# Performance work log

Measured on AMD Instinct MI355X. Metric: run time of the kernel, lower is better.

## Reference

```python
import jax, jax.numpy as jnp
import numpy as np

B, S, T, H, NH, NL = 16, 128, 64, 128, 8, 4
DH = H // NH
FF = 2 * H
SCALE = 1.0 / float(np.sqrt(DH))


def _ln(x, s, b):
    m = x.mean(-1, keepdims=True)
    v = ((x - m) ** 2).mean(-1, keepdims=True)
    return (x - m) * jax.lax.rsqrt(v + 1e-5) * s + b


def _block(x, mask, p):
    Wq, bq, Wk, bk, Wv, bv, Wo, bo, s1, c1, W1, d1, W2, d2, s2, c2 = p
    N, L, _ = x.shape
    q = (x @ Wq + bq).reshape(N, L, NH, DH)
    k = (x @ Wk + bk).reshape(N, L, NH, DH)
    v = (x @ Wv + bv).reshape(N, L, NH, DH)
    scores = jnp.einsum('nqhd,nkhd->nhqk', q, k) * SCALE
    scores = jnp.where(mask[:, None, :, :], scores, -1e9)
    a = jax.nn.softmax(scores, axis=-1)
    o = jnp.einsum('nhqk,nkhd->nqhd', a, v).reshape(N, L, H)
    x = _ln(x + o @ Wo + bo, s1, c1)
    h = jax.nn.relu(x @ W1 + d1)
    return _ln(x + h @ W2 + d2, s2, c2)


def setup_inputs():
    key = jax.random.key(0)
    ks = jax.random.split(key, 16)
    g = lambda k, shape: jax.random.normal(k, shape, jnp.float32) * 0.02
    return {
        'polylines': jax.random.normal(ks[0], (B, S, T, H), jnp.float32),
        'lengths': jax.random.randint(ks[1], (B, S), 0, T + 1),
        'proj_w': g(ks[2], (H, H)), 'proj_b': jnp.zeros((H,), jnp.float32),
        'proj_ln_s': jnp.ones((H,), jnp.float32), 'proj_ln_b': jnp.zeros((H,), jnp.float32),
        'pos_emb': g(ks[3], (1, T, H)),
        'Wq': g(ks[4], (NL, H, H)), 'bq': jnp.zeros((NL, H), jnp.float32),
        'Wk': g(ks[5], (NL, H, H)), 'bk': jnp.zeros((NL, H), jnp.float32),
        'Wv': g(ks[6], (NL, H, H)), 'bv': jnp.zeros((NL, H), jnp.float32),
        'Wo': g(ks[7], (NL, H, H)), 'bo': jnp.zeros((NL, H), jnp.float32),
        'ln1_s': jnp.ones((NL, H), jnp.float32), 'ln1_b': jnp.zeros((NL, H), jnp.float32),
        'W1': g(ks[8], (NL, H, FF)), 'b1': jnp.zeros((NL, FF), jnp.float32),
        'W2': g(ks[9], (NL, FF, H)), 'b2': jnp.zeros((NL, H), jnp.float32),
        'ln2_s': jnp.ones((NL, H), jnp.float32), 'ln2_b': jnp.zeros((NL, H), jnp.float32),
    }


def reference(polylines, lengths, proj_w, proj_b, proj_ln_s, proj_ln_b, pos_emb,
              Wq, bq, Wk, bk, Wv, bv, Wo, bo, ln1_s, ln1_b, W1, b1, W2, b2, ln2_s, ln2_b):
    # valid[b,s,t] = t < lengths[b,s]; lengths==0 -> polyline absent (fully padded)
    valid = jnp.arange(T)[None, None, :] < lengths[:, :, None]  # [B,S,T]
    x = jnp.where(valid[..., None], polylines, -1.0)            # -1 pad as in np.pad(constant_values=-1)
    # mask_temporal[b,s] = outer(valid[b,s], valid[b,s])
    mask_t = (valid[:, :, :, None] & valid[:, :, None, :]).reshape(B * S, T, T)
    # mask_spatial[b,t] = outer(valid[b,:,t], valid[b,:,t])
    vs = jnp.transpose(valid, (0, 2, 1))                        # [B,T,S]
    mask_s = (vs[:, :, :, None] & vs[:, :, None, :]).reshape(B * T, S, S)

    x = x.reshape(B * S, T, H)
    x = jax.nn.relu(_ln(x @ proj_w + proj_b, proj_ln_s, proj_ln_b))  # MLP: Linear->LN->ReLU
    x = x + pos_emb[:, :T, :]

    mask = mask_t
    for i in range(NL):
        if i == NL // 2:
            # switch from temporal to spatial attention: [B*S,T,H] -> [B*T,S,H]
            x = x.reshape(B, S, T, H).transpose(0, 2, 1, 3).reshape(B * T, S, H)
            mask = mask_s
        p = (Wq[i], bq[i], Wk[i], bk[i], Wv[i], bv[i], Wo[i], bo[i],
             ln1_s[i], ln1_b[i], W1[i], b1[i], W2[i], b2[i], ln2_s[i], ln2_b[i])
        x = _block(x, mask, p)
    # faithful to original final reshape (treats [B*T,S,H] buffer as [B,S,T,H])
    return x.reshape(B, S, T, H)[:, 0, :]
```

## Files before the change

### kernel.cpp

```cpp
#include <hip/hip_runtime.h>
#include <hip/hip_cooperative_groups.h>

namespace cg = cooperative_groups;

typedef short short8 __attribute__((ext_vector_type(8)));
typedef short short4_t __attribute__((ext_vector_type(4)));
typedef float floatx4 __attribute__((ext_vector_type(4)));
typedef unsigned short ushort_t;

#define B_ 16
#define S_ 128
#define T_ 64
#define H_ 128
#define FF_ 256
#define SCALEQK 0.25f

#define OFFP 0
#define OFFQ(l) (16384 + (l) * 65536)
#define OFFK(l) (OFFQ(l) + 16384)
#define OFFV(l) (OFFQ(l) + 32768)
#define OFFO(l) (OFFQ(l) + 49152)
#define OFFW1(l) (278528 + (l) * 65536)
#define OFFW2(l) (OFFW1(l) + 32768)

__device__ __forceinline__ float b2f(ushort_t u) {
    union { unsigned int i; float f; } x; x.i = ((unsigned int)u) << 16; return x.f;
}
__device__ __forceinline__ ushort_t f2b(float f) {
    union { float f; unsigned int i; } x; x.f = f;
    unsigned int r = x.i + 0x7fffu + ((x.i >> 16) & 1u);
    return (ushort_t)(r >> 16);
}
__device__ __forceinline__ int pack2b(float a, float b) {
    return (int)f2b(a) | ((int)f2b(b) << 16);
}

struct WtEnt { const float* src; int N; int K; int nclog2; int dstoff; };
struct WtArgs { WtEnt e[25]; };

__global__ __launch_bounds__(256) void wt_kernel(WtArgs a, ushort_t* __restrict__ dst) {
    WtEnt ent = a.e[blockIdx.x];
    const int tiles_c = ent.N >> 5;
    const int nt = (ent.K >> 5) * tiles_c;
    const int t = blockIdx.y;
    if (t >= nt) return;
    const int tc = t & (tiles_c - 1);
    const int tr = t >> ent.nclog2;
    __shared__ float ld[32 * 33];
    const int tid = threadIdx.x;
#pragma unroll
    for (int i = 0; i < 4; ++i) {
        int e = tid + i * 256;
        int rr = e >> 5, cc = e & 31;
        ld[rr * 33 + cc] = ent.src[(tr * 32 + rr) * ent.N + tc * 32 + cc];
    }
    __syncthreads();
    ushort_t* d = dst + ent.dstoff;
#pragma unroll
    for (int i = 0; i < 4; ++i) {
        int e = tid + i * 256;
        int rr = e >> 5, cc = e & 31;
        d[(tc * 32 + rr) * ent.K + tr * 32 + cc] = f2b(ld[cc * 33 + rr]);
    }
}

template<int RT, int CT, int KK>
__device__ __forceinline__ void mm_g(const ushort_t* aL, int sa,
                                     const ushort_t* __restrict__ wT,
                                     int colbase, int lane, floatx4 (&acc)[RT][CT]) {
    const int l15 = lane & 15, lq8 = (lane >> 4) * 8;
#pragma unroll
    for (int r = 0; r < RT; ++r)
#pragma unroll
        for (int c = 0; c < CT; ++c) acc[r][c] = (floatx4){0.f, 0.f, 0.f, 0.f};
#pragma unroll
    for (int k0 = 0; k0 < KK; k0 += 32) {
        short8 b[CT];
#pragma unroll
        for (int c = 0; c < CT; ++c)
            b[c] = *(const short8*)&wT[(colbase + c * 16 + l15) * KK + k0 + lq8];
#pragma unroll
        for (int r = 0; r < RT; ++r) {
            short8 a = *(const short8*)&aL[(r * 16 + l15) * sa + k0 + lq8];
#pragma unroll
            for (int c = 0; c < CT; ++c)
                acc[r][c] = __builtin_amdgcn_mfma_f32_16x16x32_bf16(a, b[c], acc[r][c], 0, 0, 0);
        }
    }
}

template<int RT, int CT>
__device__ __forceinline__ void add_bias(floatx4 (&acc)[RT][CT], const float* b,
                                         int colbase, int l15) {
#pragma unroll
    for (int c = 0; c < CT; ++c) {
        float bc = b[colbase + c * 16 + l15];
#pragma unroll
        for (int r = 0; r < RT; ++r)
#pragma unroll
            for (int g = 0; g < 4; ++g) acc[r][c][g] += bc;
    }
}

template<int RT, int CT>
__device__ __forceinline__ void add_resid_reg(floatx4 (&acc)[RT][CT],
                                              const float (&res)[RT][CT][4]) {
#pragma unroll
    for (int r = 0; r < RT; ++r)
#pragma unroll
        for (int c = 0; c < CT; ++c)
#pragma unroll
            for (int g = 0; g < 4; ++g) acc[r][c][g] += res[r][c][g];
}
template<int RT, int CT>
__device__ __forceinline__ void save_resid(float (&res)[RT][CT][4],
                                           const floatx4 (&acc)[RT][CT]) {
#pragma unroll
    for (int r = 0; r < RT; ++r)
#pragma unroll
        for (int c = 0; c < CT; ++c)
#pragma unroll
            for (int g = 0; g < 4; ++g) res[r][c][g] = acc[r][c][g];
}

template<int RT, int CT>
__device__ __forceinline__ void st_n(const floatx4 (&acc)[RT][CT], ushort_t* dst, int stride,
                                     int colbase, int l15, int lq) {
#pragma unroll
    for (int r = 0; r < RT; ++r)
#pragma unroll
        for (int g = 0; g < 4; ++g) {
            int row = r * 16 + lq * 4 + g;
#pragma unroll
            for (int c = 0; c < CT; ++c)
                dst[row * stride + colbase + c * 16 + l15] = f2b(acc[r][c][g]);
        }
}

template<int RT, int CT>
__device__ __forceinline__ void st_t(const floatx4 (&acc)[RT][CT], ushort_t* dst, int stride,
                                     int colbase, int l15, int lq) {
#pragma unroll
    for (int r = 0; r < RT; ++r)
#pragma unroll
        for (int c = 0; c < CT; ++c) {
            int d = colbase + c * 16 + l15;
            short4_t p;
#pragma unroll
            for (int g = 0; g < 4; ++g) p[g] = (short)f2b(acc[r][c][g]);
            *(short4_t*)&dst[d * stride + r * 16 + lq * 4] = p;
        }
}

template<int RT, int CT>
__device__ __forceinline__ void ln_norm(floatx4 (&acc)[RT][CT], float* redL,
                                        const float* lns, const float* lnb,
                                        int colbase, int l15, int lq, int wv) {
#pragma unroll
    for (int r = 0; r < RT; ++r)
#pragma unroll
        for (int g = 0; g < 4; ++g) {
            float s = 0.f, q = 0.f;
#pragma unroll
            for (int c = 0; c < CT; ++c) { float v = acc[r][c][g]; s += v; q += v * v; }
            s += __shfl_xor(s, 1); s += __shfl_xor(s, 2); s += __shfl_xor(s, 4); s += __shfl_xor(s, 8);
            q += __shfl_xor(q, 1); q += __shfl_xor(q, 2); q += __shfl_xor(q, 4); q += __shfl_xor(q, 8);
            if (l15 == 0) {
                int row = r * 16 + lq * 4 + g;
                redL[row * 8 + wv] = s;
                redL[row * 8 + 4 + wv] = q;
            }
        }
    __syncthreads();
#pragma unroll
    for (int r = 0; r < RT; ++r)
#pragma unroll
        for (int g = 0; g < 4; ++g) {
            int row = r * 16 + lq * 4 + g;
            float4 S = *(float4*)&redL[row * 8];
            float4 Q = *(float4*)&redL[row * 8 + 4];
            float mean = (S.x + S.y + S.z + S.w) * (1.f / 128.f);
            float var = (Q.x + Q.y + Q.z + Q.w) * (1.f / 128.f) - mean * mean;
            float rstd = rsqrtf(var + 1e-5f);
#pragma unroll
            for (int c = 0; c < CT; ++c) {
                int col = colbase + c * 16 + l15;
                acc[r][c][g] = (acc[r][c][g] - mean) * rstd * lns[col] + lnb[col];
            }
        }
}

template<int JT>
__device__ __forceinline__ void softmax_pack(floatx4 (&st)[JT], bool iv, unsigned jm,
                                             int (&px)[JT][2]) {
    float ev[JT][4];
    float mx = -3.0e38f;
#pragma unroll
    for (int jt = 0; jt < JT; ++jt)
#pragma unroll
        for (int g = 0; g < 4; ++g) {
            bool ok = iv && ((jm >> (jt * 4 + g)) & 1u);
            float s = ok ? st[jt][g] * SCALEQK : -1e9f;
            ev[jt][g] = s; mx = fmaxf(mx, s);
        }
    mx = fmaxf(mx, __shfl_xor(mx, 16)); mx = fmaxf(mx, __shfl_xor(mx, 32));
    float sum = 0.f;
#pragma unroll
    for (int jt = 0; jt < JT; ++jt)
#pragma unroll
        for (int g = 0; g < 4; ++g) { float e = __expf(ev[jt][g] - mx); ev[jt][g] = e; sum += e; }
    sum += __shfl_xor(sum, 16); sum += __shfl_xor(sum, 32);
    float inv = 1.f / sum;
#pragma unroll
    for (int jt = 0; jt < JT; ++jt) {
        px[jt][0] = pack2b(ev[jt][0] * inv, ev[jt][1] * inv);
        px[jt][1] = pack2b(ev[jt][2] * inv, ev[jt][3] * inv);
    }
}

__device__ __forceinline__ short8 pfrag(const int (*px)[2], int jc, int lq, int l15) {
    const int jA = (lq & 1) * 32 + l15;
    int a0 = __shfl(px[jc * 2][0], jA);
    int a1 = __shfl(px[jc * 2][1], jA);
    int a2 = __shfl(px[jc * 2][0], jA + 16);
    int a3 = __shfl(px[jc * 2][1], jA + 16);
    int b0 = __shfl(px[jc * 2 + 1][0], jA);
    int b1 = __shfl(px[jc * 2 + 1][1], jA);
    int b2 = __shfl(px[jc * 2 + 1][0], jA + 16);
    int b3 = __shfl(px[jc * 2 + 1][1], jA + 16);
    const bool t = (lq >> 1) != 0;
    union { int4 i; short8 s; } u;
    u.i = make_int4(t ? b0 : a0, t ? b1 : a1, t ? b2 : a2, t ? b3 : a3);
    return u.s;
}
__device__ __forceinline__ short8 vfrag(const ushort_t* vT, int stride, int row, int off) {
    int2 a = *(const int2*)&vT[row * stride + off];
    int2 b = *(const int2*)&vT[row * stride + off + 4];
    union { int4 i; short8 s; } u;
    u.i = make_int4(a.x, a.y, b.x, b.y);
    return u.s;
}

__global__ __launch_bounds__(256, 2) void k1_mega(
    const float* __restrict__ poly, const int* __restrict__ lens,
    const ushort_t* __restrict__ wt,
    const float* __restrict__ projb, const float* __restrict__ pls,
    const float* __restrict__ plb, const float* __restrict__ pos,
    const float* __restrict__ bq0, const float* __restrict__ bk0,
    const float* __restrict__ bv0, const float* __restrict__ bo0,
    const float* __restrict__ l1s0, const float* __restrict__ l1b0,
    const float* __restrict__ b10, const float* __restrict__ b20,
    const float* __restrict__ l2s0, const float* __restrict__ l2b0,
    const float* __restrict__ bq1, const float* __restrict__ bk1,
    const float* __restrict__ bv1,
    ushort_t* __restrict__ o1, float* __restrict__ xr0f)
{
    __shared__ ushort_t pool[34816];
    __shared__ float redL[512];
    __shared__ float psL[8 * 68];
    __shared__ float q1L[128];
    ushort_t* xL = pool;
    ushort_t* qL = pool + 8704;
    ushort_t* kL = pool + 17408;
    ushort_t* vT = pool + 26112;
    ushort_t* hL = pool + 17408;

    const int tid = threadIdx.x, lane = tid & 63, wv = tid >> 6;
    const int l15 = lane & 15, lq = lane >> 4;
    const int gid = blockIdx.x;
    const int len = lens[gid];

    {
        const float* pg = poly + (size_t)gid * 8192;
#pragma unroll
        for (int it = 0; it < 8; ++it) {
            int e4 = (tid + it * 256) * 4;
            int row = e4 >> 7, col = e4 & 127;
            float4 f = *(const float4*)(pg + e4);
            if (row >= len) { f.x = -1.f; f.y = -1.f; f.z = -1.f; f.w = -1.f; }
            short4_t u;
            u[0] = (short)f2b(f.x); u[1] = (short)f2b(f.y);
            u[2] = (short)f2b(f.z); u[3] = (short)f2b(f.w);
            *(short4_t*)&xL[row * 136 + col] = u;
        }
    }
    __syncthreads();

    floatx4 a2[4][2];
    float xre[4][2][4];

    mm_g<4, 2, 128>(xL, 136, wt + OFFP, wv * 32, lane, a2);
    add_bias<4, 2>(a2, projb, wv * 32, l15);
    ln_norm<4, 2>(a2, redL, pls, plb, wv * 32, l15, lq, wv);
    __syncthreads();
#pragma unroll
    for (int r = 0; r < 4; ++r)
#pragma unroll
        for (int gg = 0; gg < 4; ++gg) {
            int row = r * 16 + lq * 4 + gg;
#pragma unroll
            for (int c = 0; c < 2; ++c) {
                int col = wv * 32 + c * 16 + l15;
                float v = fmaxf(a2[r][c][gg], 0.f) + pos[row * 128 + col];
                xre[r][c][gg] = v;
                xL[row * 136 + col] = f2b(v);
            }
        }
    __syncthreads();

    mm_g<4, 2, 128>(xL, 136, wt + OFFQ(0), wv * 32, lane, a2);
    add_bias<4, 2>(a2, bq0, wv * 32, l15);
    st_n<4, 2>(a2, qL, 136, wv * 32, l15, lq);
    mm_g<4, 2, 128>(xL, 136, wt + OFFK(0), wv * 32, lane, a2);
    add_bias<4, 2>(a2, bk0, wv * 32, l15);
    st_n<4, 2>(a2, kL, 136, wv * 32, l15, lq);
    mm_g<4, 2, 128>(xL, 136, wt + OFFV(0), wv * 32, lane, a2);
    add_bias<4, 2>(a2, bv0, wv * 32, l15);
    st_t<4, 2>(a2, vT, 68, wv * 32, l15, lq);
    __syncthreads();

    {
        const int iRow = wv * 16 + l15;
        const bool iv = iRow < len;
        unsigned jm = 0;
#pragma unroll
        for (int jt = 0; jt < 4; ++jt)
#pragma unroll
            for (int gg = 0; gg < 4; ++gg)
                if (jt * 16 + lq * 4 + gg < len) jm |= (1u << (jt * 4 + gg));
        for (int h = 0; h < 8; ++h) {
            const int hc = h * 16;
            short8 z8 = {0, 0, 0, 0, 0, 0, 0, 0};
            short8 bqf = z8;
            if (lq < 2) bqf = *(const short8*)&qL[iRow * 136 + hc + lq * 8];
            floatx4 st[4];
#pragma unroll
            for (int jt = 0; jt < 4; ++jt) {
                short8 ak = z8;
                if (lq < 2) ak = *(const short8*)&kL[(jt * 16 + l15) * 136 + hc + lq * 8];
                floatx4 zz = {0.f, 0.f, 0.f, 0.f};
                st[jt] = __builtin_amdgcn_mfma_f32_16x16x32_bf16(ak, bqf, zz, 0, 0, 0);
            }
            int px[4][2];
            softmax_pack<4>(st, iv, jm, px);
            floatx4 ao = {0.f, 0.f, 0.f, 0.f};
#pragma unroll
            for (int jc = 0; jc < 2; ++jc) {
                short8 av = vfrag(vT, 68, hc + l15, jc * 32 + lq * 8);
                short8 bp = pfrag(px, jc, lq, l15);
                ao = __builtin_amdgcn_mfma_f32_16x16x32_bf16(av, bp, ao, 0, 0, 0);
            }
            short4_t w;
#pragma unroll
            for (int gg = 0; gg < 4; ++gg) w[gg] = (short)f2b(ao[gg]);
            *(short4_t*)&qL[iRow * 136 + hc + lq * 4] = w;
        }
    }
    __syncthreads();

    mm_g<4, 2, 128>(qL, 136, wt + OFFO(0), wv * 32, lane, a2);
    add_bias<4, 2>(a2, bo0, wv * 32, l15);
    add_resid_reg<4, 2>(a2, xre);
    ln_norm<4, 2>(a2, redL, l1s0, l1b0, wv * 32, l15, lq, wv);
    save_resid<4, 2>(xre, a2);
    st_n<4, 2>(a2, xL, 136, wv * 32, l15, lq);
    __syncthreads();

    {
        floatx4 a4[4][4];
        mm_g<4, 4, 128>(xL, 136, wt + OFFW1(0), wv * 64, lane, a4);
        add_bias<4, 4>(a4, b10, wv * 64, l15);
#pragma unroll
        for (int r = 0; r < 4; ++r)
#pragma unroll
            for (int c = 0; c < 4; ++c)
#pragma unroll
                for (int gg = 0; gg < 4; ++gg) a4[r][c][gg] = fmaxf(a4[r][c][gg], 0.f);
        st_n<4, 4>(a4, hL, 272, wv * 64, l15, lq);
    }
    __syncthreads();

    mm_g<4, 2, 256>(hL, 272, wt + OFFW2(0), wv * 32, lane, a2);
    add_bias<4, 2>(a2, b20, wv * 32, l15);
    add_resid_reg<4, 2>(a2, xre);
    ln_norm<4, 2>(a2, redL, l2s0, l2b0, wv * 32, l15, lq, wv);
    save_resid<4, 2>(xre, a2);
    st_n<4, 2>(a2, xL, 136, wv * 32, l15, lq);
    if (lq == 0) {
#pragma unroll
        for (int c = 0; c < 2; ++c)
            xr0f[(size_t)gid * 128 + wv * 32 + c * 16 + l15] = a2[0][c][0];
    }
    __syncthreads();

    mm_g<4, 2, 128>(xL, 136, wt + OFFK(1), wv * 32, lane, a2);
    add_bias<4, 2>(a2, bk1, wv * 32, l15);
    st_n<4, 2>(a2, kL, 136, wv * 32, l15, lq);
    mm_g<4, 2, 128>(xL, 136, wt + OFFV(1), wv * 32, lane, a2);
    add_bias<4, 2>(a2, bv1, wv * 32, l15);
    st_t<4, 2>(a2, vT, 68, wv * 32, l15, lq);
    if (tid < 128) {
        int d = tid;
        float a = bq1[d];
        const ushort_t* wq = wt + OFFQ(1) + d * 128;
#pragma unroll 4
        for (int j0 = 0; j0 < 128; j0 += 8) {
            short8 w8 = *(const short8*)&wq[j0];
            short8 x8 = *(const short8*)&xL[j0];
#pragma unroll
            for (int q = 0; q < 8; ++q)
                a = fmaf(b2f((ushort_t)x8[q]), b2f((ushort_t)w8[q]), a);
        }
        q1L[d] = a;
    }
    __syncthreads();

    {
        int h = tid >> 5, jj = tid & 31;
        int hc = h * 16;
        float s[2];
#pragma unroll
        for (int half = 0; half < 2; ++half) {
            int j = jj + half * 32;
            float a = 0.f;
            short8 k0v = *(const short8*)&kL[j * 136 + hc];
            short8 k1v = *(const short8*)&kL[j * 136 + hc + 8];
#pragma unroll
            for (int q = 0; q < 8; ++q) {
                a = fmaf(q1L[hc + q], b2f((ushort_t)k0v[q]), a);
                a = fmaf(q1L[hc + 8 + q], b2f((ushort_t)k1v[q]), a);
            }
            s[half] = (j < len) ? a * SCALEQK : -1e9f;
        }
        float mx = fmaxf(s[0], s[1]);
#pragma unroll
        for (int d = 1; d < 32; d <<= 1) mx = fmaxf(mx, __shfl_xor(mx, d));
        float e0 = __expf(s[0] - mx), e1 = __expf(s[1] - mx);
        float sum = e0 + e1;
#pragma unroll
        for (int d = 1; d < 32; d <<= 1) sum += __shfl_xor(sum, d);
        float inv = 1.f / sum;
        psL[h * 68 + jj] = e0 * inv;
        psL[h * 68 + jj + 32] = e1 * inv;
    }
    __syncthreads();
    if (tid < 128) {
        int h = tid >> 4, d = tid & 15, hc = h * 16;
        float a = 0.f;
#pragma unroll 4
        for (int j0 = 0; j0 < 64; j0 += 4) {
            float4 p4 = *(const float4*)&psL[h * 68 + j0];
            short4_t v4 = *(const short4_t*)&vT[(hc + d) * 68 + j0];
            a += p4.x * b2f((ushort_t)v4[0]) + p4.y * b2f((ushort_t)v4[1])
               + p4.z * b2f((ushort_t)v4[2]) + p4.w * b2f((ushort_t)v4[3]);
        }
        o1[(size_t)gid * 128 + hc + d] = f2b(a);
    }
}

__device__ __forceinline__ void k2a_body(char* smem, int blk,
    const ushort_t* __restrict__ xg, const int* __restrict__ lens,
    const ushort_t* __restrict__ wt, int l,
    const float* __restrict__ bq, const float* __restrict__ bk,
    const float* __restrict__ bv,
    ushort_t* __restrict__ aob)
{
    ushort_t* xL = (ushort_t*)(smem);
    ushort_t* qL = (ushort_t*)(smem + 34816);
    ushort_t* kL = (ushort_t*)(smem + 40960);
    ushort_t* vT = (ushort_t*)(smem + 47104);
    int* vldL = (int*)(smem + 51456);

    const int tid = threadIdx.x, lane = tid & 63, wv = tid >> 6;
    const int l15 = lane & 15, lq = lane >> 4;
    const int g = blk >> 3, h = blk & 7, hc = h * 16;
    const size_t rowg = (size_t)g * 128;

#pragma unroll
    for (int it = 0; it < 8; ++it) {
        int e8 = tid + it * 256;
        int row = e8 >> 4, kg = e8 & 15;
        *(short8*)&xL[row * 136 + kg * 8] = *(const short8*)&xg[(rowg + row) * 128 + kg * 8];
    }
    if (tid < 128) vldL[tid] = (lens[g * 128 + tid] > 0) ? 1 : 0;
    __syncthreads();

    unsigned jm = 0;
#pragma unroll
    for (int jt = 0; jt < 8; ++jt)
#pragma unroll
        for (int gg = 0; gg < 4; ++gg)
            if (vldL[jt * 16 + lq * 4 + gg]) jm |= (1u << (jt * 4 + gg));

    {
        floatx4 a1[2][1];
        mm_g<2, 1, 128>(xL + (wv * 32) * 136, 136, wt + OFFQ(l), hc, lane, a1);
        add_bias<2, 1>(a1, bq, hc, l15);
        st_n<2, 1>(a1, qL + (wv * 32) * 24, 24, 0, l15, lq);
        mm_g<2, 1, 128>(xL + (wv * 32) * 136, 136, wt + OFFK(l), hc, lane, a1);
        add_bias<2, 1>(a1, bk, hc, l15);
        st_n<2, 1>(a1, kL + (wv * 32) * 24, 24, 0, l15, lq);
        mm_g<2, 1, 128>(xL + (wv * 32) * 136, 136, wt + OFFV(l), hc, lane, a1);
        add_bias<2, 1>(a1, bv, hc, l15);
        st_t<2, 1>(a1, vT + wv * 32, 136, 0, l15, lq);
    }
    __syncthreads();

    for (int u = 0; u < 2; ++u) {
        const int iRow = wv * 32 + u * 16 + l15;
        const bool iv = vldL[iRow] != 0;
        short8 z8 = {0, 0, 0, 0, 0, 0, 0, 0};
        short8 bqf = z8;
        if (lq < 2) bqf = *(const short8*)&qL[iRow * 24 + lq * 8];
        floatx4 st[8];
#pragma unroll
        for (int jt = 0; jt < 8; ++jt) {
            short8 ak = z8;
            if (lq < 2) ak = *(const short8*)&kL[(jt * 16 + l15) * 24 + lq * 8];
            floatx4 zz = {0.f, 0.f, 0.f, 0.f};
            st[jt] = __builtin_amdgcn_mfma_f32_16x16x32_bf16(ak, bqf, zz, 0, 0, 0);
        }
        int px[8][2];
        softmax_pack<8>(st, iv, jm, px);
        floatx4 ao = {0.f, 0.f, 0.f, 0.f};
#pragma unroll
        for (int jc = 0; jc < 4; ++jc) {
            short8 av = vfrag(vT, 136, l15, jc * 32 + lq * 8);
            short8 bp = pfrag(px, jc, lq, l15);
            ao = __builtin_amdgcn_mfma_f32_16x16x32_bf16(av, bp, ao, 0, 0, 0);
        }
        short4_t w;
#pragma unroll
        for (int gg = 0; gg < 4; ++gg) w[gg] = (short)f2b(ao[gg]);
        *(short4_t*)&aob[(rowg + iRow) * 128 + hc + lq * 4] = w;
    }
}

template<bool FINAL>
__device__ __forceinline__ void k2b_body(char* smem, int blk,
    const ushort_t* __restrict__ ain, float* __restrict__ xr,
    const ushort_t* __restrict__ wt, int l,
    const float* bo_l, const float* l1s_l, const float* l1b_l,
    const float* b1_l, const float* b2_l, const float* l2s_l, const float* l2b_l,
    ushort_t* __restrict__ xg, float* __restrict__ outp)
{
    ushort_t* aL = (ushort_t*)(smem);
    ushort_t* hL = (ushort_t*)(smem + 4352);
    float* redL = (float*)(smem + 13056);

    const int tid = threadIdx.x, lane = tid & 63, wv = tid >> 6;
    const int l15 = lane & 15, lq = lane >> 4;
    const size_t rowbase = FINAL ? ((size_t)(blk >> 2) * 128 + (blk & 3) * 16)
                                 : ((size_t)blk * 16);

    {
        int row = tid >> 4, kg = tid & 15;
        *(short8*)&aL[row * 136 + kg * 8] = *(const short8*)&ain[(rowbase + row) * 128 + kg * 8];
    }
    __syncthreads();

    floatx4 a2[1][2];
    float xre[1][2][4];

    mm_g<1, 2, 128>(aL, 136, wt + OFFO(l), wv * 32, lane, a2);
    add_bias<1, 2>(a2, bo_l, wv * 32, l15);
#pragma unroll
    for (int c = 0; c < 2; ++c)
#pragma unroll
        for (int gg = 0; gg < 4; ++gg)
            a2[0][c][gg] += xr[(rowbase + lq * 4 + gg) * 128 + wv * 32 + c * 16 + l15];
    ln_norm<1, 2>(a2, redL, l1s_l, l1b_l, wv * 32, l15, lq, wv);
    save_resid<1, 2>(xre, a2);
    st_n<1, 2>(a2, aL, 136, wv * 32, l15, lq);
    __syncthreads();

    {
        floatx4 a4[1][4];
        mm_g<1, 4, 128>(aL, 136, wt + OFFW1(l), wv * 64, lane, a4);
        add_bias<1, 4>(a4, b1_l, wv * 64, l15);
#pragma unroll
        for (int c = 0; c < 4; ++c)
#pragma unroll
            for (int gg = 0; gg < 4; ++gg) a4[0][c][gg] = fmaxf(a4[0][c][gg], 0.f);
        st_n<1, 4>(a4, hL, 272, wv * 64, l15, lq);
    }
    __syncthreads();

    mm_g<1, 2, 256>(hL, 272, wt + OFFW2(l), wv * 32, lane, a2);
    add_bias<1, 2>(a2, b2_l, wv * 32, l15);
    add_resid_reg<1, 2>(a2, xre);
    ln_norm<1, 2>(a2, redL, l2s_l, l2b_l, wv * 32, l15, lq, wv);

    if (FINAL) {
#pragma unroll
        for (int c = 0; c < 2; ++c)
#pragma unroll
            for (int gg = 0; gg < 4; ++gg) {
                int orow = (blk >> 2) * 64 + (blk & 3) * 16 + lq * 4 + gg;
                outp[(size_t)orow * 128 + wv * 32 + c * 16 + l15] = a2[0][c][gg];
            }
    } else {
#pragma unroll
        for (int c = 0; c < 2; ++c)
#pragma unroll
            for (int gg = 0; gg < 4; ++gg) {
                size_t grow = rowbase + lq * 4 + gg;
                int col = wv * 32 + c * 16 + l15;
                float v = a2[0][c][gg];
                xg[grow * 128 + col] = f2b(v);
                xr[grow * 128 + col] = v;
            }
    }
}

__global__ __launch_bounds__(256, 1) void k2_coop(
    const ushort_t* __restrict__ o1buf, float* __restrict__ xrf,
    const int* __restrict__ lens, const ushort_t* __restrict__ wt,
    const float* __restrict__ bq, const float* __restrict__ bk,
    const float* __restrict__ bv, const float* __restrict__ bo,
    const float* __restrict__ l1s, const float* __restrict__ l1b,
    const float* __restrict__ b1, const float* __restrict__ b2,
    const float* __restrict__ l2s, const float* __restrict__ l2b,
    ushort_t* __restrict__ xg, ushort_t* __restrict__ aob,
    float* __restrict__ outp)
{
    cg::grid_group grid = cg::this_grid();
    __shared__ __align__(16) char smem[51968];
    const int blk = blockIdx.x;

    k2b_body<false>(smem, blk, o1buf, xrf, wt, 1,
                    bo + H_, l1s + H_, l1b + H_, b1 + FF_, b2 + H_, l2s + H_, l2b + H_,
                    xg, nullptr);
    grid.sync();
    k2a_body(smem, blk, xg, lens, wt, 2, bq + 2 * H_, bk + 2 * H_, bv + 2 * H_, aob);
    grid.sync();
    k2b_body<false>(smem, blk, aob, xrf, wt, 2,
                    bo + 2 * H_, l1s + 2 * H_, l1b + 2 * H_, b1 + 2 * FF_, b2 + 2 * H_,
                    l2s + 2 * H_, l2b + 2 * H_,
                    xg, nullptr);
    grid.sync();
    k2a_body(smem, blk, xg, lens, wt, 3, bq + 3 * H_, bk + 3 * H_, bv + 3 * H_, aob);
    grid.sync();
    if (blk < 64)
        k2b_body<true>(smem, blk, aob, xrf, wt, 3,
                       bo + 3 * H_, l1s + 3 * H_, l1b + 3 * H_, b1 + 3 * FF_, b2 + 3 * H_,
                       l2s + 3 * H_, l2b + 3 * H_,
                       nullptr, outp);
}

extern "C" void kernel_launch(void* const* d_in, const int* in_sizes, int n_in,
                              void* d_out, int out_size, void* d_ws, size_t ws_size,
                              hipStream_t stream)
{
    const float* poly   = (const float*)d_in[0];
    const int*   lens   = (const int*)d_in[1];
    const float* proj_w = (const float*)d_in[2];
    const float* proj_b = (const float*)d_in[3];
    const float* pls    = (const float*)d_in[4];
    const float* plb    = (const float*)d_in[5];
    const float* pos    = (const float*)d_in[6];
    const float* Wq = (const float*)d_in[7];
    const float* bq = (const float*)d_in[8];
    const float* Wk = (const float*)d_in[9];
    const float* bk = (const float*)d_in[10];
    const float* Wv = (const float*)d_in[11];
    const float* bv = (const float*)d_in[12];
    const float* Wo = (const float*)d_in[13];
    const float* bo = (const float*)d_in[14];
    const float* l1s = (const float*)d_in[15];
    const float* l1b = (const float*)d_in[16];
    const float* W1 = (const float*)d_in[17];
    const float* b1 = (const float*)d_in[18];
    const float* W2 = (const float*)d_in[19];
    const float* b2 = (const float*)d_in[20];
    const float* l2s = (const float*)d_in[21];
    const float* l2b = (const float*)d_in[22];
    float* outp = (float*)d_out;

    char* base = (char*)d_ws;
    ushort_t* wt    = (ushort_t*)base;
    ushort_t* o1buf = (ushort_t*)(base + 1081344);
    float* xrf      = (float*)(base + 1605632);
    ushort_t* xgbuf = (ushort_t*)(base + 2654208);
    ushort_t* aob   = (ushort_t*)(base + 3178496);

    const int HH = H_ * H_, HF = H_ * FF_;
    WtArgs wa;
    wa.e[0] = {proj_w, 128, 128, 2, OFFP};
    for (int l = 0; l < 4; ++l) {
        wa.e[1 + l * 4 + 0] = {Wq + l * HH, 128, 128, 2, OFFQ(l)};
        wa.e[1 + l * 4 + 1] = {Wk + l * HH, 128, 128, 2, OFFK(l)};
        wa.e[1 + l * 4 + 2] = {Wv + l * HH, 128, 128, 2, OFFV(l)};
        wa.e[1 + l * 4 + 3] = {Wo + l * HH, 128, 128, 2, OFFO(l)};
    }
    for (int l = 0; l < 4; ++l) {
        wa.e[17 + l * 2 + 0] = {W1 + l * HF, 256, 128, 3, OFFW1(l)};
        wa.e[17 + l * 2 + 1] = {W2 + l * HF, 128, 256, 2, OFFW2(l)};
    }
    wt_kernel<<<dim3(25, 32), 256, 0, stream>>>(wa, wt);

    k1_mega<<<dim3(2048), 256, 0, stream>>>(
        poly, lens, wt,
        proj_b, pls, plb, pos,
        bq, bk, bv, bo, l1s, l1b, b1, b2, l2s, l2b,
        bq + H_, bk + H_, bv + H_,
        o1buf, xrf);

    {
        const ushort_t* p0 = o1buf; float* p1 = xrf; const int* p2 = lens;
        const ushort_t* p3 = wt;
        const float* p4 = bq; const float* p5 = bk; const float* p6 = bv;
        const float* p7 = bo; const float* p8 = l1s; const float* p9 = l1b;
        const float* p10 = b1; const float* p11 = b2; const float* p12 = l2s;
        const float* p13 = l2b;
        ushort_t* p14 = xgbuf; ushort_t* p15 = aob; float* p16 = outp;
        void* kargs[] = {&p0, &p1, &p2, &p3, &p4, &p5, &p6, &p7, &p8, &p9,
                         &p10, &p11, &p12, &p13, &p14, &p15, &p16};
        hipLaunchCooperativeKernel((void*)k2_coop, dim3(128), dim3(256),
                                   kargs, 0, stream);
    }
}
```

Baseline: 451.6 us.

## Replace cooperative grid syncs with per-group atomic flag barriers

Replaces the cooperative launch and its full grid.sync calls with a normal launch where each block synchronizes only with the 8 blocks of its batch group, using atomic counters kept in workspace and cleared by a memset. This relies on spatial-attention stages depending only on blocks in the same batch, so groups no longer wait for the whole grid and the cooperative-launch overhead goes away. It adds a memset and relies on all 128 blocks being co-resident so the spin-waits cannot deadlock.

Measured after the change: 391.7 us. 13.3% less time.

```diff
diff --git a/kernel.cpp b/kernel.cpp
--- a/kernel.cpp
+++ b/kernel.cpp
@@ -1,7 +1,4 @@
 #include <hip/hip_runtime.h>
-#include <hip/hip_cooperative_groups.h>
-
-namespace cg = cooperative_groups;
 
 typedef short short8 __attribute__((ext_vector_type(8)));
 typedef short short4_t __attribute__((ext_vector_type(4)));
@@ -613,7 +610,21 @@
     }
 }
 
-__global__ __launch_bounds__(256, 1) void k2_coop(
+__device__ __forceinline__ void sync_group(unsigned* pf, int idx, unsigned target, int tid) {
+    __syncthreads();
+    if (tid == 0) {
+        __threadfence();
+        __hip_atomic_fetch_add(&pf[idx * 16], 1u, __ATOMIC_RELEASE,
+                               __HIP_MEMORY_SCOPE_AGENT);
+        while (__hip_atomic_load(&pf[idx * 16], __ATOMIC_ACQUIRE,
+                                 __HIP_MEMORY_SCOPE_AGENT) < target)
+            __builtin_amdgcn_s_sleep(8);
+        __threadfence();
+    }
+    __syncthreads();
+}
+
+__global__ __launch_bounds__(256) void k3_tail(
     const ushort_t* __restrict__ o1buf, float* __restrict__ xrf,
     const int* __restrict__ lens, const ushort_t* __restrict__ wt,
     const float* __restrict__ bq, const float* __restrict__ bk,
@@ -622,27 +633,32 @@
     const float* __restrict__ b1, const float* __restrict__ b2,
     const float* __restrict__ l2s, const float* __restrict__ l2b,
     ushort_t* __restrict__ xg, ushort_t* __restrict__ aob,
-    float* __restrict__ outp)
+    float* __restrict__ outp, unsigned* __restrict__ pf)
 {
-    cg::grid_group grid = cg::this_grid();
     __shared__ __align__(16) char smem[51968];
-    const int blk = blockIdx.x;
-
-    k2b_body<false>(smem, blk, o1buf, xrf, wt, 1,
+    const int t = (int)blockIdx.x;
+    const int g = t >> 3, sub = t & 7;
+    const int tid = threadIdx.x;
+
+    k2b_body<false>(smem, t, o1buf, xrf, wt, 1,
                     bo + H_, l1s + H_, l1b + H_, b1 + FF_, b2 + H_, l2s + H_, l2b + H_,
                     xg, nullptr);
-    grid.sync();
-    k2a_body(smem, blk, xg, lens, wt, 2, bq + 2 * H_, bk + 2 * H_, bv + 2 * H_, aob);
-    grid.sync();
-    k2b_body<false>(smem, blk, aob, xrf, wt, 2,
+    sync_group(pf, g * 4 + 0, 8, tid);
+
+    k2a_body(smem, t, xg, lens, wt, 2, bq + 2 * H_, bk + 2 * H_, bv + 2 * H_, aob);
+    sync_group(pf, g * 4 + 1, 8, tid);
+
+    k2b_body<false>(smem, t, aob, xrf, wt, 2,
                     bo + 2 * H_, l1s + 2 * H_, l1b + 2 * H_, b1 + 2 * FF_, b2 + 2 * H_,
                     l2s + 2 * H_, l2b + 2 * H_,
                     xg, nullptr);
-    grid.sync();
-    k2a_body(smem, blk, xg, lens, wt, 3, bq + 3 * H_, bk + 3 * H_, bv + 3 * H_, aob);
-    grid.sync();
-    if (blk < 64)
-        k2b_body<true>(smem, blk, aob, xrf, wt, 3,
+    sync_group(pf, g * 4 + 2, 8, tid);
+
+    k2a_body(smem, t, xg, lens, wt, 3, bq + 3 * H_, bk + 3 * H_, bv + 3 * H_, aob);
+    sync_group(pf, g * 4 + 3, 8, tid);
+
+    if (sub < 4)
+        k2b_body<true>(smem, g * 4 + sub, aob, xrf, wt, 3,
                        bo + 3 * H_, l1s + 3 * H_, l1b + 3 * H_, b1 + 3 * FF_, b2 + 3 * H_,
                        l2s + 3 * H_, l2b + 3 * H_,
                        nullptr, outp);
@@ -683,6 +699,9 @@
     float* xrf      = (float*)(base + 1605632);
     ushort_t* xgbuf = (ushort_t*)(base + 2654208);
     ushort_t* aob   = (ushort_t*)(base + 3178496);
+    unsigned* pf    = (unsigned*)(base + 3702784);
+
+    hipMemsetAsync(pf, 0, 64 * 64, stream);
 
     const int HH = H_ * H_, HF = H_ * FF_;
     WtArgs wa;
@@ -706,17 +725,8 @@
         bq + H_, bk + H_, bv + H_,
         o1buf, xrf);
 
-    {
-        const ushort_t* p0 = o1buf; float* p1 = xrf; const int* p2 = lens;
-        const ushort_t* p3 = wt;
-        const float* p4 = bq; const float* p5 = bk; const float* p6 = bv;
-        const float* p7 = bo; const float* p8 = l1s; const float* p9 = l1b;
-        const float* p10 = b1; const float* p11 = b2; const float* p12 = l2s;
-        const float* p13 = l2b;
-        ushort_t* p14 = xgbuf; ushort_t* p15 = aob; float* p16 = outp;
-        void* kargs[] = {&p0, &p1, &p2, &p3, &p4, &p5, &p6, &p7, &p8, &p9,
-                         &p10, &p11, &p12, &p13, &p14, &p15, &p16};
-        hipLaunchCooperativeKernel((void*)k2_coop, dim3(128), dim3(256),
-                                   kargs, 0, stream);
-    }
-}
+    k3_tail<<<dim3(128), 256, 0, stream>>>(
+        o1buf, xrf, lens, wt,
+        bq, bk, bv, bo, l1s, l1b, b1, b2, l2s, l2b,
+        xgbuf, aob, outp, pf);
+}
```
